# Kernel tuning notes

Hardware: AMD Instinct MI355X
Metric: run time of the kernel (lower is better)

## Reference

```python
import jax, jax.numpy as jnp
import numpy as np

B, S, D = 2, 2048, 2048
H, HD = 16, 128
ROPE_THETA = 10000.0


def _rope_cos_sin(seq_len, head_dim, dtype=jnp.float32):
    inv_freq = 1.0 / (ROPE_THETA ** (jnp.arange(0, head_dim, 2, dtype=jnp.float32) / head_dim))
    t = jnp.arange(seq_len, dtype=jnp.float32)
    freqs = jnp.outer(t, inv_freq)                     # [S, HD/2]
    emb = jnp.concatenate([freqs, freqs], axis=-1)     # [S, HD]
    return jnp.cos(emb).astype(dtype), jnp.sin(emb).astype(dtype)


def _rotate_half(x):
    x1, x2 = jnp.split(x, 2, axis=-1)
    return jnp.concatenate([-x2, x1], axis=-1)


def _apply_rope(x, cos, sin):
    # x: [B, S, H, HD]; cos/sin: [S, HD] -> broadcast over batch and heads
    c = cos[None, :, None, :]
    s = sin[None, :, None, :]
    return x * c + _rotate_half(x) * s


def setup_inputs() -> dict:
    key = jax.random.key(0)
    ks = jax.random.split(key, 6)
    scale = 1.0 / np.sqrt(D)
    hidden_states = jax.random.normal(ks[0], (B, S, D), dtype=jnp.float32)
    # causal additive mask: 0 on/below diagonal, large negative above
    neg = jnp.finfo(jnp.float32).min
    causal = jnp.where(jnp.tril(jnp.ones((S, S), dtype=bool)), 0.0, neg)
    attention_mask = jnp.broadcast_to(causal[None, None, :, :], (B, 1, S, S)).astype(jnp.float32)
    Wq = jax.random.normal(ks[1], (D, D), dtype=jnp.float32) * scale
    Wk = jax.random.normal(ks[2], (D, D), dtype=jnp.float32) * scale
    Wv = jax.random.normal(ks[3], (D, D), dtype=jnp.float32) * scale
    Wo = jax.random.normal(ks[4], (D, D), dtype=jnp.float32) * scale
    return {"hidden_states": hidden_states, "attention_mask": attention_mask,
            "Wq": Wq, "Wk": Wk, "Wv": Wv, "Wo": Wo}


def reference(hidden_states, attention_mask, Wq, Wk, Wv, Wo):
    b, s, d = hidden_states.shape
    # projections (torch Linear: x @ W^T)
    q = (hidden_states @ Wq.T).reshape(b, s, H, HD)
    k = (hidden_states @ Wk.T).reshape(b, s, H, HD)
    v = (hidden_states @ Wv.T).reshape(b, s, H, HD)
    cos, sin = _rope_cos_sin(s, HD, hidden_states.dtype)
    q = _apply_rope(q, cos, sin)
    k = _apply_rope(k, cos, sin)
    # naive attention, [B, H, S, S] scores materialized as in the original
    scores = jnp.einsum('bqhd,bkhd->bhqk', q, k) / np.sqrt(HD)
    scores = scores + attention_mask
    attn = jax.nn.softmax(scores, axis=-1)
    out = jnp.einsum('bhqk,bkhd->bqhd', attn, v).reshape(b, s, d)
    return out @ Wo.T
```

## Files before the change

### kernel.cpp

```cpp
#include <hip/hip_runtime.h>
#include <hip/hip_bf16.h>

typedef __hip_bfloat16 bf16;
typedef __attribute__((ext_vector_type(8))) short s16x8;
typedef __attribute__((ext_vector_type(4))) float f32x4;
typedef __attribute__((ext_vector_type(16))) float f32x16;

#define MFMA16(a, b, c) __builtin_amdgcn_mfma_f32_16x16x32_bf16(a, b, c, 0, 0, 0)
#define MFMA32(a, b, c) __builtin_amdgcn_mfma_f32_32x32x16_bf16(a, b, c, 0, 0, 0)

#define GLL16(gsrc, ldst)                                                                 \
  __builtin_amdgcn_global_load_lds(                                                       \
      (const __attribute__((address_space(1))) unsigned int*)(gsrc),                      \
      (__attribute__((address_space(3))) unsigned int*)(ldst), 16, 0, 0)

#define VMCNT(n) asm volatile("s_waitcnt vmcnt(" #n ")" ::: "memory")
#define BARRIER() __builtin_amdgcn_s_barrier()

static constexpr int S_LEN = 2048;
static constexpr int D_DIM = 2048;
static constexpr int NY = 6144;

union BF4 { ushort4 u; bf16 b[4]; };

__device__ inline unsigned pack2(float a, float b) {
  union { bf16 h[2]; unsigned u; } x;
  x.h[0] = __float2bfloat16(a);
  x.h[1] = __float2bfloat16(b);
  return x.u;
}

__global__ void convert_kernel(const float* __restrict__ src, bf16* __restrict__ dst, int n) {
  int i = (blockIdx.x * blockDim.x + threadIdx.x) * 4;
  if (i >= n) return;
  float4 v = *(const float4*)(src + i);
  BF4 o;
  o.b[0] = __float2bfloat16(v.x);
  o.b[1] = __float2bfloat16(v.y);
  o.b[2] = __float2bfloat16(v.z);
  o.b[3] = __float2bfloat16(v.w);
  *(ushort4*)(dst + i) = o.u;
}

__global__ void trig_kernel(float* __restrict__ cosT, float* __restrict__ sinT) {
  int i = blockIdx.x * blockDim.x + threadIdx.x;
  int d = i & 63, s = i >> 6;
  float inv = powf(10000.0f, -(float)d * (1.0f / 64.0f));
  float ang = (float)s * inv;
  cosT[i] = cosf(ang);
  sinT[i] = sinf(ang);
}

__global__ void rope_kernel(bf16* __restrict__ Y, const float* __restrict__ cosT,
                            const float* __restrict__ sinT) {
  int idx = blockIdx.x * blockDim.x + threadIdx.x;
  int quad = idx & 15;
  int h = (idx >> 4) & 15;
  int m = (idx >> 8) & 4095;
  int g = idx >> 20;
  int s = m & (S_LEN - 1);
  int d0 = quad * 4;
  float sc = g ? 1.0f : 0.08838834764831845f;
  bf16* p = Y + (size_t)m * NY + g * D_DIM + h * 128 + d0;
  BF4 lo, hi, olo, ohi;
  lo.u = *(const ushort4*)p;
  hi.u = *(const ushort4*)(p + 64);
  float4 c = *(const float4*)(cosT + s * 64 + d0);
  float4 sn = *(const float4*)(sinT + s * 64 + d0);
  float cc[4] = {c.x, c.y, c.z, c.w};
  float ss[4] = {sn.x, sn.y, sn.z, sn.w};
#pragma unroll
  for (int i = 0; i < 4; ++i) {
    float x1 = __bfloat162float(lo.b[i]);
    float x2 = __bfloat162float(hi.b[i]);
    olo.b[i] = __float2bfloat16((x1 * cc[i] - x2 * ss[i]) * sc);
    ohi.b[i] = __float2bfloat16((x2 * cc[i] + x1 * ss[i]) * sc);
  }
  *(ushort4*)p = olo.u;
  *(ushort4*)(p + 64) = ohi.u;
}

__global__ __launch_bounds__(256) void transpose_v(const bf16* __restrict__ Y,
                                                   bf16* __restrict__ Vt) {
  __shared__ bf16 tile[32][36];
  int bh = blockIdx.z;
  int b = bh >> 4, h = bh & 15;
  int s0 = blockIdx.x * 32, d0 = blockIdx.y * 32;
  int t = threadIdx.x;
  int r = t >> 3;
  int c4 = (t & 7) * 4;
  BF4 in;
  in.u = *(const ushort4*)(Y + (size_t)(b * S_LEN + s0 + r) * NY + 4096 + h * 128 + d0 + c4);
  *(ushort4*)(&tile[r][c4]) = in.u;
  __syncthreads();
  BF4 o;
#pragma unroll
  for (int i = 0; i < 4; ++i) o.b[i] = tile[c4 + i][r];
  *(ushort4*)(Vt + (size_t)bh * 128 * S_LEN + (size_t)(d0 + r) * S_LEN + s0 + c4) = o.u;
}

__device__ inline void storeC(float* p, float v) { *p = v; }
__device__ inline void storeC(bf16* p, float v) { *p = __float2bfloat16(v); }


__device__ __forceinline__ void stage_tileA(const bf16* gA, int lda, int k0, char* dstA,
                                            int w, int lane) {
  int rl = w * 8 + (lane >> 3);
  int sc = ((lane & 7) ^ ((lane >> 3) & 7)) << 3;
  const bf16* s0 = gA + (size_t)rl * lda + k0 + sc;
  GLL16(s0, dstA + w * 1024);
  GLL16(s0 + (size_t)64 * lda, dstA + 8192 + w * 1024);
}

__device__ __forceinline__ void stage_tileB(const bf16* gB, int ldb, int k0, char* dstB,
                                            int w, int lane) {
  int rl = w * 8 + (lane >> 3);
  int sc = ((lane & 7) ^ ((lane >> 3) & 7)) << 3;
  const bf16* s0 = gB + (size_t)rl * ldb + k0 + sc;
#pragma unroll
  for (int c = 0; c < 4; ++c) GLL16(s0 + (size_t)(c * 64) * ldb, dstB + c * 8192 + w * 1024);
}

template <typename OutT>
__global__ __launch_bounds__(512, 2) void gemm8p(const bf16* __restrict__ A,
                                                 const bf16* __restrict__ Bm,
                                                 OutT* __restrict__ C, int K, int lda, int ldb,
                                                 int ldc, int mt) {
  __shared__ __align__(16) char lds[98304];
  const int tid = threadIdx.x;
  const int lane = tid & 63;
  const int w = tid >> 6;
  const int wm = w >> 2, wn = w & 3;
  const int l15 = lane & 15, lh4 = lane >> 4;
  const int xr = (l15 & 7);

  const int nwg = gridDim.x;
  const int bid = blockIdx.x;
  const int swz = (bid & 7) * (nwg >> 3) + (bid >> 3);
  const int bm = swz % mt, bn = swz / mt;
  const int row0 = bm * 128, col0 = bn * 256;

  const bf16* gA = A + (size_t)row0 * lda;
  const bf16* gB = Bm + (size_t)col0 * ldb;
  char* bufA0 = lds;
  char* bufB0 = lds + 16384;
  char* bufA1 = lds + 49152;
  char* bufB1 = lds + 49152 + 16384;

  f32x4 acc[4][4];
#pragma unroll
  for (int i = 0; i < 4; ++i)
#pragma unroll
    for (int j = 0; j < 4; ++j) acc[i][j] = (f32x4){0.f, 0.f, 0.f, 0.f};

  s16x8 bfr[4][2];
  s16x8 af[2][2];

  stage_tileB(gB, ldb, 0, bufB0, w, lane);
  stage_tileA(gA, lda, 0, bufA0, w, lane);
  stage_tileB(gB, ldb, 64, bufB1, w, lane);
  VMCNT(4);
  BARRIER();

#define READ_A(buf, rh)                                                                    \
  _Pragma("unroll") for (int ii = 0; ii < 2; ++ii) _Pragma("unroll") for (int ks = 0;      \
                                                                          ks < 2; ++ks)    \
      af[ii][ks] = *(const s16x8*)((buf) + (wm * 64 + (rh)*32 + ii * 16 + l15) * 128 +     \
                                   (((ks * 4 + lh4) ^ xr) << 4));
#define READ_B(buf)                                                                        \
  _Pragma("unroll") for (int j = 0; j < 4; ++j) _Pragma("unroll") for (int ks = 0; ks < 2; \
                                                                       ++ks) bfr[j][ks] =  \
      *(const s16x8*)((buf) + (wn * 64 + j * 16 + l15) * 128 + (((ks * 4 + lh4) ^ xr) << 4));
#define MFMA_BLK(rh)                                                                       \
  __builtin_amdgcn_s_setprio(1);                                                           \
  _Pragma("unroll") for (int j = 0; j < 4; ++j) _Pragma("unroll") for (int ii = 0; ii < 2; \
                                                                       ++ii)               \
      _Pragma("unroll") for (int ks = 0; ks < 2; ++ks) acc[(rh)*2 + ii][j] =               \
          MFMA16(af[ii][ks], bfr[j][ks], acc[(rh)*2 + ii][j]);                             \
  __builtin_amdgcn_s_setprio(0);

  const int NI = K >> 7;
  for (int i = 0; i < NI; ++i) {
    const bool nl = (i + 1 < NI);
    READ_A(bufA0, 0);
    READ_B(bufB0);
    stage_tileA(gA, lda, (2 * i + 1) * 64, bufA1, w, lane);
    BARRIER();
    MFMA_BLK(0);
    BARRIER();
    READ_A(bufA0, 1);
    if (nl) stage_tileB(gB, ldb, (2 * i + 2) * 64, bufB0, w, lane);
    BARRIER();
    MFMA_BLK(1);
    if (nl) { VMCNT(4); } else { VMCNT(0); }
    BARRIER();
    READ_A(bufA1, 0);
    READ_B(bufB1);
    if (nl) stage_tileA(gA, lda, (2 * i + 2) * 64, bufA0, w, lane);
    BARRIER();
    MFMA_BLK(0);
    BARRIER();
    READ_A(bufA1, 1);
    if (nl) stage_tileB(gB, ldb, (2 * i + 3) * 64, bufB1, w, lane);
    BARRIER();
    MFMA_BLK(1);
    if (nl) { VMCNT(4); }
    BARRIER();
  }
#undef READ_A
#undef READ_B
#undef MFMA_BLK

#pragma unroll
  for (int mi = 0; mi < 4; ++mi)
#pragma unroll
    for (int ni = 0; ni < 4; ++ni) {
      int gr = row0 + wm * 64 + mi * 16 + lh4 * 4;
      int gc = col0 + wn * 64 + ni * 16 + l15;
#pragma unroll
      for (int rr = 0; rr < 4; ++rr)
        storeC(&C[(size_t)(gr + rr) * ldc + gc], acc[mi][ni][rr]);
    }
}

__global__ __launch_bounds__(256, 2) void attn_fwd(const bf16* __restrict__ Y,
                                                   const bf16* __restrict__ Vt,
                                                   bf16* __restrict__ At) {
  __shared__ __align__(16) char smem[32768];
  bf16* Ks = (bf16*)smem;
  bf16* Vs = (bf16*)(smem + 16384);

  const int idx = blockIdx.x;
  const int qt = 15 - (idx >> 5);
  const int bh = idx & 31;
  const int b = bh >> 4, h = bh & 15;
  const int tid = threadIdx.x;
  const int lane = tid & 63;
  const int w = tid >> 6;
  const int l31 = lane & 31;
  const int hi = lane >> 5;
  const int q0w = qt * 128 + w * 32;
  const int q = q0w + l31;

  s16x8 qf[8];
  {
    const bf16* qb = Y + (size_t)(b * S_LEN + q) * NY + h * 128 + hi * 8;
#pragma unroll
    for (int s = 0; s < 8; ++s) qf[s] = *(const s16x8*)(qb + s * 16);
  }

  f32x16 O[4];
#pragma unroll
  for (int d = 0; d < 4; ++d)
#pragma unroll
    for (int e = 0; e < 16; ++e) O[d][e] = 0.f;
  float m_run = -3.0e38f, l_run = 0.f;

  const bf16* Kbase = Y + (size_t)(b * S_LEN) * NY + 2048 + h * 128;
  const bf16* Vbase = Vt + (size_t)bh * 128 * S_LEN;
  const int tmax = 2 * qt + 1;

  for (int t = 0; t <= tmax; ++t) {
    const int kv0 = t * 64;
    __syncthreads();
#pragma unroll
    for (int j = 0; j < 4; ++j) {
      int rk = j * 16 + w * 4 + (lane >> 4);
      int ck = lane & 15;
      GLL16(Kbase + (size_t)(kv0 + rk) * NY + ((ck ^ (rk & 15)) * 8),
            Ks + (j * 2048 + w * 512));
      int dv = j * 32 + w * 8 + (lane >> 3);
      int cv = lane & 7;
      GLL16(Vbase + (size_t)dv * S_LEN + kv0 + ((cv ^ (dv & 7)) * 8),
            Vs + (j * 2048 + w * 512));
    }
    __syncthreads();
    if (kv0 > q0w + 31) continue;

    float sv[32];
#pragma unroll
    for (int tt = 0; tt < 2; ++tt) {
      f32x16 sa;
#pragma unroll
      for (int e = 0; e < 16; ++e) sa[e] = 0.f;
      const int rk = tt * 32 + l31;
      const char* kr = (const char*)Ks + rk * 256;
      const int xr = (rk & 15) << 4;
#pragma unroll
      for (int s = 0; s < 8; ++s) {
        s16x8 kf = *(const s16x8*)(kr + ((s * 32 + hi * 16) ^ xr));
        sa = MFMA32(kf, qf[s], sa);
      }
#pragma unroll
      for (int e = 0; e < 16; ++e) sv[tt * 16 + e] = sa[e];
    }

    if (kv0 + 63 > q0w) {
#pragma unroll
      for (int tt = 0; tt < 2; ++tt)
#pragma unroll
        for (int r = 0; r < 16; ++r) {
          int kvr = kv0 + tt * 32 + (r & 3) + 8 * (r >> 2) + 4 * hi;
          if (kvr > q) sv[tt * 16 + r] = -3.0e38f;
        }
    }

    float mx[16];
#pragma unroll
    for (int i = 0; i < 16; ++i) mx[i] = fmaxf(sv[i], sv[i + 16]);
#pragma unroll
    for (int st = 8; st >= 1; st >>= 1)
#pragma unroll
      for (int i = 0; i < 8; ++i)
        if (i < st) mx[i] = fmaxf(mx[i], mx[i + st]);
    float pmax = fmaxf(mx[0], __shfl_xor(mx[0], 32, 64));

    bool need = pmax > m_run + 8.0f;
    if (__any(need)) {
      float newm = fmaxf(m_run, pmax);
      float ef = __expf(m_run - newm);
      m_run = newm;
      l_run *= ef;
#pragma unroll
      for (int d = 0; d < 4; ++d)
#pragma unroll
        for (int e = 0; e < 16; ++e) O[d][e] *= ef;
    }

    float rsum = 0.f;
#pragma unroll
    for (int i = 0; i < 32; ++i) {
      sv[i] = __expf(sv[i] - m_run);
      rsum += sv[i];
    }
    rsum += __shfl_xor(rsum, 32, 64);
    l_run += rsum;

    unsigned pw[4][4];
#pragma unroll
    for (int tt = 0; tt < 2; ++tt) {
      const int bs = tt * 16;
      unsigned x01 = pack2(sv[bs + 0], sv[bs + 1]);
      unsigned x23 = pack2(sv[bs + 2], sv[bs + 3]);
      unsigned x45 = pack2(sv[bs + 4], sv[bs + 5]);
      unsigned x67 = pack2(sv[bs + 6], sv[bs + 7]);
      unsigned y01 = pack2(sv[bs + 8], sv[bs + 9]);
      unsigned y23 = pack2(sv[bs + 10], sv[bs + 11]);
      unsigned y45 = pack2(sv[bs + 12], sv[bs + 13]);
      unsigned y67 = pack2(sv[bs + 14], sv[bs + 15]);
      unsigned sx01 = __shfl_xor(x01, 32, 64), sx23 = __shfl_xor(x23, 32, 64);
      unsigned sx45 = __shfl_xor(x45, 32, 64), sx67 = __shfl_xor(x67, 32, 64);
      unsigned sy01 = __shfl_xor(y01, 32, 64), sy23 = __shfl_xor(y23, 32, 64);
      unsigned sy45 = __shfl_xor(y45, 32, 64), sy67 = __shfl_xor(y67, 32, 64);
      pw[tt * 2][0] = hi ? sx45 : x01;
      pw[tt * 2][1] = hi ? sx67 : x23;
      pw[tt * 2][2] = hi ? x45 : sx01;
      pw[tt * 2][3] = hi ? x67 : sx23;
      pw[tt * 2 + 1][0] = hi ? sy45 : y01;
      pw[tt * 2 + 1][1] = hi ? sy67 : y23;
      pw[tt * 2 + 1][2] = hi ? y45 : sy01;
      pw[tt * 2 + 1][3] = hi ? y67 : sy23;
    }

#pragma unroll
    for (int dt = 0; dt < 4; ++dt) {
      const int d = dt * 32 + l31;
      const char* vr = (const char*)Vs + d * 128;
      const int xv = (d & 7) << 4;
#pragma unroll
      for (int sl = 0; sl < 4; ++sl) {
        s16x8 vf = *(const s16x8*)(vr + ((sl * 32 + hi * 16) ^ xv));
        union { unsigned u[4]; s16x8 v; } pb;
        pb.u[0] = pw[sl][0];
        pb.u[1] = pw[sl][1];
        pb.u[2] = pw[sl][2];
        pb.u[3] = pw[sl][3];
        O[dt] = MFMA32(vf, pb.v, O[dt]);
      }
    }
  }

  __syncthreads();
  const float inv = 1.0f / l_run;
  {
    const int orow = w * 32 + l31;
    const int xo = (orow & 15) << 4;
    char* obase = (char*)smem + orow * 256;
#pragma unroll
    for (int dt = 0; dt < 4; ++dt)
#pragma unroll
      for (int r = 0; r < 16; ++r) {
        int d = dt * 32 + (r & 3) + 8 * (r >> 2) + 4 * hi;
        *(bf16*)(obase + ((d * 2) ^ xo)) = __float2bfloat16(O[dt][r] * inv);
      }
  }
  __syncthreads();
  bf16* dst = At + (size_t)(b * S_LEN + qt * 128) * D_DIM + h * 128;
#pragma unroll
  for (int j = 0; j < 8; ++j) {
    int id = j * 256 + tid;
    int rr = id >> 4, cc = id & 15;
    int4 val = *(const int4*)((char*)smem + rr * 256 + ((cc * 16) ^ ((rr & 15) << 4)));
    *(int4*)(dst + (size_t)rr * D_DIM + cc * 8) = val;
  }
}

extern "C" void kernel_launch(void* const* d_in, const int* in_sizes, int n_in,
                              void* d_out, int out_size, void* d_ws, size_t ws_size,
                              hipStream_t stream) {
  const float* X = (const float*)d_in[0];
  const float* Wq = (const float*)d_in[2];
  const float* Wk = (const float*)d_in[3];
  const float* Wv = (const float*)d_in[4];
  const float* Wo = (const float*)d_in[5];
  float* out = (float*)d_out;
  char* ws = (char*)d_ws;

  bf16* Xb = (bf16*)(ws);
  bf16* Wb = (bf16*)(ws + 16777216);
  bf16* Wob = (bf16*)(ws + 41943040);
  bf16* Y = (bf16*)(ws + 50331648);
  bf16* Vt = (bf16*)(ws + 100663296);
  bf16* At = (bf16*)(ws + 117440512);
  float* cosT = (float*)(ws + 134217728);
  float* sinT = (float*)(ws + 134742016);

  convert_kernel<<<8192, 256, 0, stream>>>(X, Xb, 8388608);
  convert_kernel<<<4096, 256, 0, stream>>>(Wq, Wb, 4194304);
  convert_kernel<<<4096, 256, 0, stream>>>(Wk, Wb + 4194304, 4194304);
  convert_kernel<<<4096, 256, 0, stream>>>(Wv, Wb + 8388608, 4194304);
  convert_kernel<<<4096, 256, 0, stream>>>(Wo, Wob, 4194304);
  trig_kernel<<<512, 256, 0, stream>>>(cosT, sinT);

  gemm8p<bf16><<<768, 512, 0, stream>>>(Xb, Wb, Y, 2048, 2048, 2048, 6144, 32);
  rope_kernel<<<8192, 256, 0, stream>>>(Y, cosT, sinT);
  transpose_v<<<dim3(64, 4, 32), 256, 0, stream>>>(Y, Vt);
  attn_fwd<<<dim3(512), 256, 0, stream>>>(Y, Vt, At);
  gemm8p<float><<<256, 512, 0, stream>>>(At, Wob, out, 2048, 2048, 2048, 2048, 32);
}
```

Measured before the change: 270.3 us.

## Add 256x256-tile ping-pong GEMM kernel for fused QKV projection

Adds a new bf16 GEMM kernel with 256x256 output tiles and double-buffered 128KB LDS, staged through direct global-to-LDS loads. The main loop is split into quarter-tile MFMA phases interleaved with loads, and uses s_setprio to favour the MFMA bursts. It replaces the earlier gemm8p launch for the QKV projection (384 blocks instead of 768), aiming for more data reuse per tile and better overlap of loads with compute. The cost is fewer workgroups and heavy LDS use, which limits occupancy and can leave CUs unevenly loaded.

```diff
diff --git a/kernel.cpp b/kernel.cpp
--- a/kernel.cpp
+++ b/kernel.cpp
@@ -102,6 +102,157 @@
 __device__ inline void storeC(float* p, float v) { *p = v; }
 __device__ inline void storeC(bf16* p, float v) { *p = __float2bfloat16(v); }
 
+__global__ __launch_bounds__(512, 2) void gemm256(const bf16* __restrict__ A,
+                                                  const bf16* __restrict__ Bm,
+                                                  bf16* __restrict__ C, int K, int lda,
+                                                  int ldb, int ldc, int mt) {
+  __shared__ __align__(16) char lds[131072];
+  char* A0buf = lds;
+  char* B0buf = lds + 32768;
+  char* A1buf = lds + 65536;
+  char* B1buf = lds + 98304;
+  const int tid = threadIdx.x;
+  const int lane = tid & 63;
+  const int w = tid >> 6;
+  const int wm = w >> 2, wn = w & 3;
+  const int l15 = lane & 15, lh4 = lane >> 4;
+  const int xr = l15 & 7;
+  const int xo0 = ((lh4 ^ xr) << 4);
+  const int xo1 = (((4 + lh4) ^ xr) << 4);
+
+  const int nwg = gridDim.x;
+  const int bid = blockIdx.x;
+  const int swz = (bid & 7) * (nwg >> 3) + (bid >> 3);
+  const int bm = swz % mt, bn = swz / mt;
+  const int row0 = bm * 256, col0 = bn * 256;
+
+  const int srow8 = lane >> 3;
+  const int scol = ((lane & 7) ^ srow8) * 8;
+  const bf16* gA_s = A + (size_t)(row0 + w * 8 + srow8) * lda + scol;
+  const bf16* gB_s = Bm + (size_t)(col0 + (w >> 2) * 64 + (w & 3) * 8 + srow8) * ldb + scol;
+  const int ldst = w * 1024;
+
+#define STAGE_A(bufa, rh, k0)                                                     \
+  {                                                                               \
+    GLL16(gA_s + (size_t)((rh)*64) * lda + (k0), (bufa) + (rh)*16384 + ldst);     \
+    GLL16(gA_s + (size_t)((rh)*64 + 128) * lda + (k0),                            \
+          (bufa) + (rh)*16384 + 8192 + ldst);                                     \
+  }
+#define STAGE_B(bufb, ch, k0)                                                     \
+  {                                                                               \
+    GLL16(gB_s + (size_t)((ch)*32) * ldb + (k0), (bufb) + (ch)*16384 + ldst);     \
+    GLL16(gB_s + (size_t)((ch)*32 + 128) * ldb + (k0),                            \
+          (bufb) + (ch)*16384 + 8192 + ldst);                                     \
+  }
+
+  f32x4 acc[8][4];
+#pragma unroll
+  for (int i = 0; i < 8; ++i)
+#pragma unroll
+    for (int j = 0; j < 4; ++j) acc[i][j] = (f32x4){0.f, 0.f, 0.f, 0.f};
+
+  s16x8 af[4][2];
+  s16x8 bfr[2][2];
+
+#define READ_AH(bufa, rh)                                                         \
+  _Pragma("unroll") for (int ii = 0; ii < 4; ++ii) {                              \
+    const char* p_ = (bufa) + (rh)*16384 + (wm * 64 + ii * 16 + l15) * 128;       \
+    af[ii][0] = *(const s16x8*)(p_ + xo0);                                        \
+    af[ii][1] = *(const s16x8*)(p_ + xo1);                                        \
+  }
+#define READ_BH(bufb, ch)                                                         \
+  _Pragma("unroll") for (int jj = 0; jj < 2; ++jj) {                              \
+    const char* p_ = (bufb) + (ch)*16384 + (wn * 32 + jj * 16 + l15) * 128;       \
+    bfr[jj][0] = *(const s16x8*)(p_ + xo0);                                       \
+    bfr[jj][1] = *(const s16x8*)(p_ + xo1);                                       \
+  }
+#define QUAD(rh, ch)                                                              \
+  __builtin_amdgcn_s_setprio(1);                                                  \
+  _Pragma("unroll") for (int jj = 0; jj < 2; ++jj)                                \
+  _Pragma("unroll") for (int ii = 0; ii < 4; ++ii)                                \
+  _Pragma("unroll") for (int ks = 0; ks < 2; ++ks)                                \
+      acc[(rh)*4 + ii][(ch)*2 + jj] =                                             \
+          MFMA16(af[ii][ks], bfr[jj][ks], acc[(rh)*4 + ii][(ch)*2 + jj]);         \
+  __builtin_amdgcn_s_setprio(0);
+
+  STAGE_A(A0buf, 0, 0);
+  STAGE_B(B0buf, 0, 0);
+  STAGE_B(B0buf, 1, 0);
+  STAGE_A(A0buf, 1, 0);
+  STAGE_A(A1buf, 0, 64);
+  STAGE_B(B1buf, 1, 64);
+  STAGE_A(A1buf, 1, 64);
+  VMCNT(6);
+  BARRIER();
+
+  const int NI = K >> 7;
+  for (int i = 0; i < NI; ++i) {
+    const int kT1 = (2 * i + 1) << 6;
+    const int kT2 = (2 * i + 2) << 6;
+    const int kT3 = (2 * i + 3) << 6;
+    const bool nl = (i + 1 < NI);
+    READ_AH(A0buf, 0);
+    READ_BH(B0buf, 0);
+    STAGE_B(B1buf, 0, kT1);
+    BARRIER();
+    QUAD(0, 0);
+    BARRIER();
+    READ_BH(B0buf, 1);
+    if (nl) STAGE_A(A0buf, 0, kT2);
+    BARRIER();
+    QUAD(0, 1);
+    BARRIER();
+    READ_AH(A0buf, 1);
+    if (nl) STAGE_B(B0buf, 1, kT2);
+    BARRIER();
+    QUAD(1, 1);
+    BARRIER();
+    READ_BH(B0buf, 0);
+    if (nl) STAGE_A(A0buf, 1, kT2);
+    BARRIER();
+    QUAD(1, 0);
+    if (nl) { VMCNT(6); } else { VMCNT(0); }
+    BARRIER();
+    READ_AH(A1buf, 0);
+    READ_BH(B1buf, 0);
+    if (nl) STAGE_B(B0buf, 0, kT2);
+    BARRIER();
+    QUAD(0, 0);
+    BARRIER();
+    READ_BH(B1buf, 1);
+    if (nl) STAGE_A(A1buf, 0, kT3);
+    BARRIER();
+    QUAD(0, 1);
+    BARRIER();
+    READ_AH(A1buf, 1);
+    if (nl) STAGE_B(B1buf, 1, kT3);
+    BARRIER();
+    QUAD(1, 1);
+    BARRIER();
+    READ_BH(B1buf, 0);
+    if (nl) STAGE_A(A1buf, 1, kT3);
+    BARRIER();
+    QUAD(1, 0);
+    if (nl) { VMCNT(6); }
+    BARRIER();
+  }
+#undef STAGE_A
+#undef STAGE_B
+#undef READ_AH
+#undef READ_BH
+#undef QUAD
+
+#pragma unroll
+  for (int ri = 0; ri < 8; ++ri)
+#pragma unroll
+    for (int cj = 0; cj < 4; ++cj) {
+      int gr = row0 + wm * 128 + ri * 16 + lh4 * 4;
+      int gc = col0 + wn * 64 + cj * 16 + l15;
+#pragma unroll
+      for (int rr = 0; rr < 4; ++rr)
+        C[(size_t)(gr + rr) * ldc + gc] = __float2bfloat16(acc[ri][cj][rr]);
+    }
+}
 
 __device__ __forceinline__ void stage_tileA(const bf16* gA, int lda, int k0, char* dstA,
                                             int w, int lane) {
@@ -432,7 +583,7 @@
   convert_kernel<<<4096, 256, 0, stream>>>(Wo, Wob, 4194304);
   trig_kernel<<<512, 256, 0, stream>>>(cosT, sinT);
 
-  gemm8p<bf16><<<768, 512, 0, stream>>>(Xb, Wb, Y, 2048, 2048, 2048, 6144, 32);
+  gemm256<<<384, 512, 0, stream>>>(Xb, Wb, Y, 2048, 2048, 2048, 6144, 16);
   rope_kernel<<<8192, 256, 0, stream>>>(Y, cosT, sinT);
   transpose_v<<<dim3(64, 4, 32), 256, 0, stream>>>(Y, Vt);
   attn_fwd<<<dim3(512), 256, 0, stream>>>(Y, Vt, At);
```

New measurement: 277.0 us. 2.5% more time.
